# Optimization experiments

Hardware: AMD Instinct MI355X
Metric: run time of the kernel (lower is better)

## Reference

```python
import jax, jax.numpy as jnp
import numpy as np

EPS = 1e-6  # epsilon used to snap near-zero plane distances (Moller-style robustness)


def _interval(p, d):
    """Interval of the intersection line covered by a triangle.
    p: [..., 3] projections of the 3 vertices onto the intersection-line axis.
    d: [..., 3] signed distances of the 3 vertices to the other triangle's plane.
    Returns (tmin, tmax); invalid (non-straddling) -> (+inf, -inf).
    """
    nxt = jnp.array([1, 2, 0])
    di, dj = d, d[..., nxt]
    pi, pj = p, p[..., nxt]
    # edge crosses the plane iff endpoint distances have opposite signs
    # (or exactly one endpoint lies on the plane)
    valid = (di * dj <= 0) & ~((di == 0) & (dj == 0))
    denom = di - dj
    t = pi + (pj - pi) * di / jnp.where(denom == 0, 1.0, denom)
    tmin = jnp.min(jnp.where(valid, t, jnp.inf), axis=-1)
    tmax = jnp.max(jnp.where(valid, t, -jnp.inf), axis=-1)
    return tmin, tmax


def _pairwise_intersect(T):
    """Moller-style triangle-triangle intersection test for all N^2 pairs.
    T: [N, 3, 3] triangle soup. Returns bool [N, N].
    """
    N = T.shape[0]
    n = jnp.cross(T[:, 1] - T[:, 0], T[:, 2] - T[:, 0])   # [N,3] plane normals
    d = -jnp.sum(n * T[:, 0], axis=-1)                      # [N] plane offsets
    # signed distances: verts of triangle b to plane of triangle u (dv), and vice versa (du)
    dv = jnp.einsum('bvc,nc->bnv', T, n) + d[None, :, None]  # [N,N,3]
    du = jnp.einsum('nvc,bc->bnv', T, n) + d[:, None, None]  # [N,N,3]
    dv = jnp.where(jnp.abs(dv) < EPS, 0.0, dv)
    du = jnp.where(jnp.abs(du) < EPS, 0.0, du)
    # all vertices strictly on one side -> no intersection
    ssv = jnp.all(dv > 0, -1) | jnp.all(dv < 0, -1)
    ssu = jnp.all(du > 0, -1) | jnp.all(du < 0, -1)
    # direction of plane-plane intersection line; project onto its dominant axis
    D = jnp.cross(n[:, None, :], n[None, :, :])              # [N,N,3]
    ax = jnp.argmax(jnp.abs(D), axis=-1)                     # [N,N]
    idx = jnp.broadcast_to(ax[..., None, None], (N, N, 3, 1))
    pv = jnp.take_along_axis(jnp.broadcast_to(T[:, None], (N, N, 3, 3)), idx, -1)[..., 0]
    pu = jnp.take_along_axis(jnp.broadcast_to(T[None, :], (N, N, 3, 3)), idx, -1)[..., 0]
    t0v, t1v = _interval(pv, dv)
    t0u, t1u = _interval(pu, du)
    overlap = jnp.maximum(t0v, t0u) <= jnp.minimum(t1v, t1u)
    return ~ssv & ~ssu & overlap


def setup_inputs() -> dict:
    key = jax.random.key(0)
    triangles = jax.random.normal(key, (2048, 3, 3), dtype=jnp.float32)
    return {"triangles": triangles}


def reference(triangles):
    # CPU extension produces the strictly-upper-triangular pairwise matrix;
    # the torch wrapper symmetrizes it and adds the identity.
    N = triangles.shape[0]
    M = _pairwise_intersect(triangles).astype(jnp.float32)
    S = jnp.triu(M, 1)
    return S + S.T + jnp.eye(N, dtype=jnp.float32)
```

## Files before the change

### kernel.cpp

```cpp
#include <hip/hip_runtime.h>
#include <math.h>


static constexpr float EPS_SNAP = 1e-6f;
static constexpr int TS = 32;

__device__ __forceinline__ float snapz(float x) {
    return (fabsf(x) < EPS_SNAP) ? 0.0f : x;
}

__device__ __forceinline__ void tri_interval(const float p[3], const float d[3],
                                             float& tmin, float& tmax) {
#pragma clang fp contract(off)
    tmin = INFINITY;
    tmax = -INFINITY;
#pragma unroll
    for (int e = 0; e < 3; ++e) {
        const int i0 = e;
        const int i1 = (e + 1) % 3;
        const float di = d[i0], dj = d[i1];
        const float pi = p[i0], pj = p[i1];
        const bool valid = (di * dj <= 0.0f) && !((di == 0.0f) && (dj == 0.0f));
        const float denom = di - dj;
        const float dsafe = (denom == 0.0f) ? 1.0f : denom;
        const float t = pi + ((pj - pi) * di) / dsafe;
        if (valid) {
            tmin = fminf(tmin, t);
            tmax = fmaxf(tmax, t);
        }
    }
}

__global__ __launch_bounds__(256) void plane_kernel(
    const float* __restrict__ tri, float4* __restrict__ planes, int n)
{
#pragma clang fp contract(off)
    const int i = blockIdx.x * 256 + threadIdx.x;
    if (i >= n) return;
    const float* A = tri + (size_t)i * 9;
    float Av[9];
#pragma unroll
    for (int k = 0; k < 9; ++k) Av[k] = A[k];
    const float e1x = Av[3] - Av[0], e1y = Av[4] - Av[1], e1z = Av[5] - Av[2];
    const float e2x = Av[6] - Av[0], e2y = Av[7] - Av[1], e2z = Av[8] - Av[2];
    const float nx = e1y * e2z - e1z * e2y;
    const float ny = e1z * e2x - e1x * e2z;
    const float nz = e1x * e2y - e1y * e2x;
    const float d = -(((nx * Av[0]) + (ny * Av[1])) + (nz * Av[2]));
    planes[i] = make_float4(nx, ny, nz, d);
}

__global__ __launch_bounds__(256) void tile_kernel(
    const float* __restrict__ tri, const float4* __restrict__ planes,
    float* __restrict__ out, int n)
{
#pragma clang fp contract(off)
    const int tc = blockIdx.x, tr = blockIdx.y;
    if (tr > tc) return;
    const int C = tc * TS, R = tr * TS;

    __shared__ float As[TS][13];
    __shared__ float Sres[TS][TS + 1];

    const int tx = threadIdx.x;
    const int t = threadIdx.y * 32 + tx;

    if (t < TS) {
        const float* a = tri + (size_t)(R + t) * 9;
#pragma unroll
        for (int k = 0; k < 9; ++k) As[t][k] = a[k];
        const float4 p = planes[R + t];
        As[t][9] = p.x; As[t][10] = p.y; As[t][11] = p.z; As[t][12] = p.w;
    }

    const int j = C + tx;
    const float* b = tri + (size_t)j * 9;
    float Bv[9];
#pragma unroll
    for (int k = 0; k < 9; ++k) Bv[k] = b[k];
    const float4 pb = planes[j];
    const float nbx = pb.x, nby = pb.y, nbz = pb.z, db = pb.w;

    __syncthreads();

#pragma unroll
    for (int kk = 0; kk < 4; ++kk) {
        const int r = threadIdx.y + 8 * kk;
        const int i = R + r;

        float Av[9];
#pragma unroll
        for (int k = 0; k < 9; ++k) Av[k] = As[r][k];
        const float nax = As[r][9], nay = As[r][10], naz = As[r][11], da = As[r][12];

        float dv[3], du[3];
#pragma unroll
        for (int v = 0; v < 3; ++v) {
            dv[v] = snapz((((Av[3 * v] * nbx) + (Av[3 * v + 1] * nby)) + (Av[3 * v + 2] * nbz)) + db);
            du[v] = snapz((((Bv[3 * v] * nax) + (Bv[3 * v + 1] * nay)) + (Bv[3 * v + 2] * naz)) + da);
        }

        const bool ssv = (dv[0] > 0.0f && dv[1] > 0.0f && dv[2] > 0.0f) ||
                         (dv[0] < 0.0f && dv[1] < 0.0f && dv[2] < 0.0f);
        const bool ssu = (du[0] > 0.0f && du[1] > 0.0f && du[2] > 0.0f) ||
                         (du[0] < 0.0f && du[1] < 0.0f && du[2] < 0.0f);

        const float Dx = nay * nbz - naz * nby;
        const float Dy = naz * nbx - nax * nbz;
        const float Dz = nax * nby - nay * nbx;
        const float m0 = fabsf(Dx), m1 = fabsf(Dy), m2 = fabsf(Dz);
        int axm = 0;
        float mm = m0;
        if (m1 > mm) { axm = 1; mm = m1; }
        if (m2 > mm) { axm = 2; }

        float pv[3], pu[3];
#pragma unroll
        for (int v = 0; v < 3; ++v) {
            pv[v] = (axm == 0) ? Av[3 * v] : ((axm == 1) ? Av[3 * v + 1] : Av[3 * v + 2]);
            pu[v] = (axm == 0) ? Bv[3 * v] : ((axm == 1) ? Bv[3 * v + 1] : Bv[3 * v + 2]);
        }

        float t0v, t1v, t0u, t1u;
        tri_interval(pv, dv, t0v, t1v);
        tri_interval(pu, du, t0u, t1u);

        const bool overlap = fmaxf(t0v, t0u) <= fminf(t1v, t1u);
        const bool hit = (!ssv) && (!ssu) && overlap;

        float res = hit ? 1.0f : 0.0f;
        if (i == j) res = 1.0f;
        Sres[r][tx] = res;
    }

    __syncthreads();

    {
        const int row = t >> 3;
        const int c4 = (t & 7) * 4;
        float4 v;
        v.x = Sres[row][c4 + 0]; v.y = Sres[row][c4 + 1];
        v.z = Sres[row][c4 + 2]; v.w = Sres[row][c4 + 3];
        *(float4*)&out[(size_t)(R + row) * n + C + c4] = v;
        if (tr != tc) {
            float4 w;
            w.x = Sres[c4 + 0][row]; w.y = Sres[c4 + 1][row];
            w.z = Sres[c4 + 2][row]; w.w = Sres[c4 + 3][row];
            *(float4*)&out[(size_t)(C + row) * n + R + c4] = w;
        }
    }
}

extern "C" void kernel_launch(void* const* d_in, const int* in_sizes, int n_in,
                              void* d_out, int out_size, void* d_ws, size_t ws_size,
                              hipStream_t stream) {
    const float* tri = (const float*)d_in[0];
    float* out = (float*)d_out;
    const int n = in_sizes[0] / 9;
    float4* planes = (float4*)d_ws;

    plane_kernel<<<(n + 255) / 256, 256, 0, stream>>>(tri, planes, n);

    dim3 block(32, 8);
    dim3 grid(n / TS, n / TS);
    tile_kernel<<<grid, block, 0, stream>>>(tri, planes, out, n);
}
```

Baseline: 78.63 us.

## Use 32x32 thread blocks with one pair per thread and scalar stores

Each tile block grows from 32x8 threads looping over four rows to 32x32 threads that each handle a single triangle pair. The direct tile is stored with per-thread scalar writes, and the mirrored tile goes through shared memory only on off-diagonal blocks. The aim is more parallelism per block and no per-thread row loop, at the cost of each thread redundantly loading B triangle data, scalar instead of float4 stores, and a __syncthreads inside a block-uniform branch.

Result: slower. 80.22 us (+2.0%).

```diff
diff --git a/kernel.cpp b/kernel.cpp
--- a/kernel.cpp
+++ b/kernel.cpp
@@ -50,7 +50,7 @@
     planes[i] = make_float4(nx, ny, nz, d);
 }
 
-__global__ __launch_bounds__(256) void tile_kernel(
+__global__ __launch_bounds__(1024) void tile_kernel(
     const float* __restrict__ tri, const float4* __restrict__ planes,
     float* __restrict__ out, int n)
 {
@@ -63,14 +63,14 @@
     __shared__ float Sres[TS][TS + 1];
 
     const int tx = threadIdx.x;
-    const int t = threadIdx.y * 32 + tx;
+    const int ty = threadIdx.y;
 
-    if (t < TS) {
-        const float* a = tri + (size_t)(R + t) * 9;
+    if (ty == 0) {
+        const float* a = tri + (size_t)(R + tx) * 9;
 #pragma unroll
-        for (int k = 0; k < 9; ++k) As[t][k] = a[k];
-        const float4 p = planes[R + t];
-        As[t][9] = p.x; As[t][10] = p.y; As[t][11] = p.z; As[t][12] = p.w;
+        for (int k = 0; k < 9; ++k) As[tx][k] = a[k];
+        const float4 p = planes[R + tx];
+        As[tx][9] = p.x; As[tx][10] = p.y; As[tx][11] = p.z; As[tx][12] = p.w;
     }
 
     const int j = C + tx;
@@ -83,71 +83,56 @@
 
     __syncthreads();
 
+    const int i = R + ty;
+    float Av[9];
 #pragma unroll
-    for (int kk = 0; kk < 4; ++kk) {
-        const int r = threadIdx.y + 8 * kk;
-        const int i = R + r;
+    for (int k = 0; k < 9; ++k) Av[k] = As[ty][k];
+    const float nax = As[ty][9], nay = As[ty][10], naz = As[ty][11], da = As[ty][12];
 
-        float Av[9];
+    float dv[3], du[3];
 #pragma unroll
-        for (int k = 0; k < 9; ++k) Av[k] = As[r][k];
-        const float nax = As[r][9], nay = As[r][10], naz = As[r][11], da = As[r][12];
-
-        float dv[3], du[3];
-#pragma unroll
-        for (int v = 0; v < 3; ++v) {
-            dv[v] = snapz((((Av[3 * v] * nbx) + (Av[3 * v + 1] * nby)) + (Av[3 * v + 2] * nbz)) + db);
-            du[v] = snapz((((Bv[3 * v] * nax) + (Bv[3 * v + 1] * nay)) + (Bv[3 * v + 2] * naz)) + da);
-        }
-
-        const bool ssv = (dv[0] > 0.0f && dv[1] > 0.0f && dv[2] > 0.0f) ||
-                         (dv[0] < 0.0f && dv[1] < 0.0f && dv[2] < 0.0f);
-        const bool ssu = (du[0] > 0.0f && du[1] > 0.0f && du[2] > 0.0f) ||
-                         (du[0] < 0.0f && du[1] < 0.0f && du[2] < 0.0f);
-
-        const float Dx = nay * nbz - naz * nby;
-        const float Dy = naz * nbx - nax * nbz;
-        const float Dz = nax * nby - nay * nbx;
-        const float m0 = fabsf(Dx), m1 = fabsf(Dy), m2 = fabsf(Dz);
-        int axm = 0;
-        float mm = m0;
-        if (m1 > mm) { axm = 1; mm = m1; }
-        if (m2 > mm) { axm = 2; }
-
-        float pv[3], pu[3];
-#pragma unroll
-        for (int v = 0; v < 3; ++v) {
-            pv[v] = (axm == 0) ? Av[3 * v] : ((axm == 1) ? Av[3 * v + 1] : Av[3 * v + 2]);
-            pu[v] = (axm == 0) ? Bv[3 * v] : ((axm == 1) ? Bv[3 * v + 1] : Bv[3 * v + 2]);
-        }
-
-        float t0v, t1v, t0u, t1u;
-        tri_interval(pv, dv, t0v, t1v);
-        tri_interval(pu, du, t0u, t1u);
-
-        const bool overlap = fmaxf(t0v, t0u) <= fminf(t1v, t1u);
-        const bool hit = (!ssv) && (!ssu) && overlap;
-
-        float res = hit ? 1.0f : 0.0f;
-        if (i == j) res = 1.0f;
-        Sres[r][tx] = res;
+    for (int v = 0; v < 3; ++v) {
+        dv[v] = snapz((((Av[3 * v] * nbx) + (Av[3 * v + 1] * nby)) + (Av[3 * v + 2] * nbz)) + db);
+        du[v] = snapz((((Bv[3 * v] * nax) + (Bv[3 * v + 1] * nay)) + (Bv[3 * v + 2] * naz)) + da);
     }
 
-    __syncthreads();
+    const bool ssv = (dv[0] > 0.0f && dv[1] > 0.0f && dv[2] > 0.0f) ||
+                     (dv[0] < 0.0f && dv[1] < 0.0f && dv[2] < 0.0f);
+    const bool ssu = (du[0] > 0.0f && du[1] > 0.0f && du[2] > 0.0f) ||
+                     (du[0] < 0.0f && du[1] < 0.0f && du[2] < 0.0f);
 
-    {
-        const int row = t >> 3;
-        const int c4 = (t & 7) * 4;
-        float4 v;
-        v.x = Sres[row][c4 + 0]; v.y = Sres[row][c4 + 1];
-        v.z = Sres[row][c4 + 2]; v.w = Sres[row][c4 + 3];
-        *(float4*)&out[(size_t)(R + row) * n + C + c4] = v;
-        if (tr != tc) {
-            float4 w;
-            w.x = Sres[c4 + 0][row]; w.y = Sres[c4 + 1][row];
-            w.z = Sres[c4 + 2][row]; w.w = Sres[c4 + 3][row];
-            *(float4*)&out[(size_t)(C + row) * n + R + c4] = w;
-        }
+    const float Dx = nay * nbz - naz * nby;
+    const float Dy = naz * nbx - nax * nbz;
+    const float Dz = nax * nby - nay * nbx;
+    const float m0 = fabsf(Dx), m1 = fabsf(Dy), m2 = fabsf(Dz);
+    int axm = 0;
+    float mm = m0;
+    if (m1 > mm) { axm = 1; mm = m1; }
+    if (m2 > mm) { axm = 2; }
+
+    float pv[3], pu[3];
+#pragma unroll
+    for (int v = 0; v < 3; ++v) {
+        pv[v] = (axm == 0) ? Av[3 * v] : ((axm == 1) ? Av[3 * v + 1] : Av[3 * v + 2]);
+        pu[v] = (axm == 0) ? Bv[3 * v] : ((axm == 1) ? Bv[3 * v + 1] : Bv[3 * v + 2]);
+    }
+
+    float t0v, t1v, t0u, t1u;
+    tri_interval(pv, dv, t0v, t1v);
+    tri_interval(pu, du, t0u, t1u);
+
+    const bool overlap = fmaxf(t0v, t0u) <= fminf(t1v, t1u);
+    const bool hit = (!ssv) && (!ssu) && overlap;
+
+    float res = hit ? 1.0f : 0.0f;
+    if (i == j) res = 1.0f;
+
+    out[(size_t)i * n + j] = res;
+
+    if (tr != tc) {
+        Sres[ty][tx] = res;
+        __syncthreads();
+        out[(size_t)(C + ty) * n + (R + tx)] = Sres[tx][ty];
     }
 }
 
@@ -161,7 +146,7 @@
 
     plane_kernel<<<(n + 255) / 256, 256, 0, stream>>>(tri, planes, n);
 
-    dim3 block(32, 8);
+    dim3 block(TS, TS);
     dim3 grid(n / TS, n / TS);
     tile_kernel<<<grid, block, 0, stream>>>(tri, planes, out, n);
 }
```

## Fuse plane computation, launch only upper tiles, compact survivors before interval test

Applied to the files above, without the earlier changes.

Plane normals are now computed inside the tile kernel from triangles staged in shared memory, so the separate plane kernel launch goes away. The grid launches only upper-triangular tiles, decoding the tile index with a loop, which removes the empty blocks that used to exit early. A cheap same-side rejection pass uses ballot and a shared atomic to compact surviving pairs into a queue. The full interval test then runs only on those survivors, reducing divergent work, at the cost of extra barriers, atomics and shared memory.

Measured after the change: 73.88 us. 6.0% less time.

```diff
diff --git a/kernel.cpp b/kernel.cpp
--- a/kernel.cpp
+++ b/kernel.cpp
@@ -31,79 +31,124 @@
     }
 }
 
-__global__ __launch_bounds__(256) void plane_kernel(
-    const float* __restrict__ tri, float4* __restrict__ planes, int n)
+__global__ __launch_bounds__(256, 4) void tile_kernel(
+    const float* __restrict__ tri, float* __restrict__ out, int n)
 {
 #pragma clang fp contract(off)
-    const int i = blockIdx.x * 256 + threadIdx.x;
-    if (i >= n) return;
-    const float* A = tri + (size_t)i * 9;
-    float Av[9];
-#pragma unroll
-    for (int k = 0; k < 9; ++k) Av[k] = A[k];
-    const float e1x = Av[3] - Av[0], e1y = Av[4] - Av[1], e1z = Av[5] - Av[2];
-    const float e2x = Av[6] - Av[0], e2y = Av[7] - Av[1], e2z = Av[8] - Av[2];
-    const float nx = e1y * e2z - e1z * e2y;
-    const float ny = e1z * e2x - e1x * e2z;
-    const float nz = e1x * e2y - e1y * e2x;
-    const float d = -(((nx * Av[0]) + (ny * Av[1])) + (nz * Av[2]));
-    planes[i] = make_float4(nx, ny, nz, d);
-}
-
-__global__ __launch_bounds__(256) void tile_kernel(
-    const float* __restrict__ tri, const float4* __restrict__ planes,
-    float* __restrict__ out, int n)
-{
-#pragma clang fp contract(off)
-    const int tc = blockIdx.x, tr = blockIdx.y;
-    if (tr > tc) return;
-    const int C = tc * TS, R = tr * TS;
-
-    __shared__ float As[TS][13];
+    const int nt = n / TS;
+    int k = blockIdx.x, tr = 0;
+    while (k >= nt - tr) { k -= nt - tr; ++tr; }
+    const int tc = tr + k;
+    const int R = tr * TS, C = tc * TS;
+
+    __shared__ float Asf[TS * 12];
+    __shared__ float Bsf[TS * 12];
+    __shared__ float4 Apl[TS], Bpl[TS];
     __shared__ float Sres[TS][TS + 1];
+    __shared__ unsigned short qbuf[TS * TS];
+    __shared__ int s_cnt;
 
     const int tx = threadIdx.x;
-    const int t = threadIdx.y * 32 + tx;
-
-    if (t < TS) {
-        const float* a = tri + (size_t)(R + t) * 9;
-#pragma unroll
-        for (int k = 0; k < 9; ++k) As[t][k] = a[k];
-        const float4 p = planes[R + t];
-        As[t][9] = p.x; As[t][10] = p.y; As[t][11] = p.z; As[t][12] = p.w;
-    }
-
-    const int j = C + tx;
-    const float* b = tri + (size_t)j * 9;
+    const int ty = threadIdx.y;
+    const int t = ty * TS + tx;
+    const int lane = t & 63;
+
+    if (t == 0) s_cnt = 0;
+    for (int g = t; g < TS * 9; g += 256) {
+        const int a = g / 9, c9 = g - a * 9;
+        Asf[a * 12 + c9] = tri[(size_t)R * 9 + g];
+        Bsf[a * 12 + c9] = tri[(size_t)C * 9 + g];
+    }
+    for (int g = t; g < TS * (TS + 1); g += 256) ((float*)Sres)[g] = 0.0f;
+    __syncthreads();
+
+    if (t < 2 * TS) {
+        const float* V = (t < TS) ? &Asf[t * 12] : &Bsf[(t - TS) * 12];
+        const float e1x = V[3] - V[0], e1y = V[4] - V[1], e1z = V[5] - V[2];
+        const float e2x = V[6] - V[0], e2y = V[7] - V[1], e2z = V[8] - V[2];
+        const float nx = e1y * e2z - e1z * e2y;
+        const float ny = e1z * e2x - e1x * e2z;
+        const float nz = e1x * e2y - e1y * e2x;
+        const float d = -(((nx * V[0]) + (ny * V[1])) + (nz * V[2]));
+        if (t < TS) Apl[t] = make_float4(nx, ny, nz, d);
+        else        Bpl[t - TS] = make_float4(nx, ny, nz, d);
+    }
+    if (tr == tc && t < TS) Sres[t][t] = 1.0f;
+    __syncthreads();
+
     float Bv[9];
-#pragma unroll
-    for (int k = 0; k < 9; ++k) Bv[k] = b[k];
-    const float4 pb = planes[j];
-    const float nbx = pb.x, nby = pb.y, nbz = pb.z, db = pb.w;
-
-    __syncthreads();
-
-#pragma unroll
+    {
+        const float4 b0 = *(const float4*)&Bsf[tx * 12];
+        const float4 b1 = *(const float4*)&Bsf[tx * 12 + 4];
+        const float4 b2 = *(const float4*)&Bsf[tx * 12 + 8];
+        Bv[0] = b0.x; Bv[1] = b0.y; Bv[2] = b0.z; Bv[3] = b0.w;
+        Bv[4] = b1.x; Bv[5] = b1.y; Bv[6] = b1.z; Bv[7] = b1.w;
+        Bv[8] = b2.x;
+    }
+    const float4 pb = Bpl[tx];
+
     for (int kk = 0; kk < 4; ++kk) {
-        const int r = threadIdx.y + 8 * kk;
-        const int i = R + r;
-
-        float Av[9];
-#pragma unroll
-        for (int k = 0; k < 9; ++k) Av[k] = As[r][k];
-        const float nax = As[r][9], nay = As[r][10], naz = As[r][11], da = As[r][12];
+        const int r = ty + 8 * kk;
+        const float4 a0 = *(const float4*)&Asf[r * 12];
+        const float4 a1 = *(const float4*)&Asf[r * 12 + 4];
+        const float4 a2 = *(const float4*)&Asf[r * 12 + 8];
+        const float4 pa = Apl[r];
+        const float dv0 = snapz((((a0.x * pb.x) + (a0.y * pb.y)) + (a0.z * pb.z)) + pb.w);
+        const float dv1 = snapz((((a0.w * pb.x) + (a1.x * pb.y)) + (a1.y * pb.z)) + pb.w);
+        const float dv2 = snapz((((a1.z * pb.x) + (a1.w * pb.y)) + (a2.x * pb.z)) + pb.w);
+        const float du0 = snapz((((Bv[0] * pa.x) + (Bv[1] * pa.y)) + (Bv[2] * pa.z)) + pa.w);
+        const float du1 = snapz((((Bv[3] * pa.x) + (Bv[4] * pa.y)) + (Bv[5] * pa.z)) + pa.w);
+        const float du2 = snapz((((Bv[6] * pa.x) + (Bv[7] * pa.y)) + (Bv[8] * pa.z)) + pa.w);
+        const float mnv = fminf(fminf(dv0, dv1), dv2), mxv = fmaxf(fmaxf(dv0, dv1), dv2);
+        const float mnu = fminf(fminf(du0, du1), du2), mxu = fmaxf(fmaxf(du0, du1), du2);
+        const bool ssv = (mnv > 0.0f) || (mxv < 0.0f);
+        const bool ssu = (mnu > 0.0f) || (mxu < 0.0f);
+        const bool surv = !ssv && !ssu && ((R + r) != (C + tx));
+        const unsigned long long m = __ballot(surv);
+        int wb = 0;
+        if (lane == 0) {
+            const int wcnt = __popcll(m);
+            if (wcnt) wb = atomicAdd(&s_cnt, wcnt);
+        }
+        wb = __shfl(wb, 0);
+        if (surv) {
+            const int pos = wb + __popcll(m & ((1ull << lane) - 1ull));
+            qbuf[pos] = (unsigned short)((r << 5) | tx);
+        }
+    }
+    __syncthreads();
+
+    const int total = s_cnt;
+    for (int q = t; q < total; q += 256) {
+        const int e = qbuf[q];
+        const int r = e >> 5, c = e & 31;
+
+        float Av[9], Bw[9];
+        {
+            const float4 a0 = *(const float4*)&Asf[r * 12];
+            const float4 a1 = *(const float4*)&Asf[r * 12 + 4];
+            const float4 a2 = *(const float4*)&Asf[r * 12 + 8];
+            Av[0] = a0.x; Av[1] = a0.y; Av[2] = a0.z; Av[3] = a0.w;
+            Av[4] = a1.x; Av[5] = a1.y; Av[6] = a1.z; Av[7] = a1.w;
+            Av[8] = a2.x;
+            const float4 b0 = *(const float4*)&Bsf[c * 12];
+            const float4 b1 = *(const float4*)&Bsf[c * 12 + 4];
+            const float4 b2 = *(const float4*)&Bsf[c * 12 + 8];
+            Bw[0] = b0.x; Bw[1] = b0.y; Bw[2] = b0.z; Bw[3] = b0.w;
+            Bw[4] = b1.x; Bw[5] = b1.y; Bw[6] = b1.z; Bw[7] = b1.w;
+            Bw[8] = b2.x;
+        }
+        const float4 pa = Apl[r];
+        const float4 pq = Bpl[c];
+        const float nax = pa.x, nay = pa.y, naz = pa.z, da = pa.w;
+        const float nbx = pq.x, nby = pq.y, nbz = pq.z, db = pq.w;
 
         float dv[3], du[3];
 #pragma unroll
         for (int v = 0; v < 3; ++v) {
             dv[v] = snapz((((Av[3 * v] * nbx) + (Av[3 * v + 1] * nby)) + (Av[3 * v + 2] * nbz)) + db);
-            du[v] = snapz((((Bv[3 * v] * nax) + (Bv[3 * v + 1] * nay)) + (Bv[3 * v + 2] * naz)) + da);
-        }
-
-        const bool ssv = (dv[0] > 0.0f && dv[1] > 0.0f && dv[2] > 0.0f) ||
-                         (dv[0] < 0.0f && dv[1] < 0.0f && dv[2] < 0.0f);
-        const bool ssu = (du[0] > 0.0f && du[1] > 0.0f && du[2] > 0.0f) ||
-                         (du[0] < 0.0f && du[1] < 0.0f && du[2] < 0.0f);
+            du[v] = snapz((((Bw[3 * v] * nax) + (Bw[3 * v + 1] * nay)) + (Bw[3 * v + 2] * naz)) + da);
+        }
 
         const float Dx = nay * nbz - naz * nby;
         const float Dy = naz * nbx - nax * nbz;
@@ -118,7 +163,7 @@
 #pragma unroll
         for (int v = 0; v < 3; ++v) {
             pv[v] = (axm == 0) ? Av[3 * v] : ((axm == 1) ? Av[3 * v + 1] : Av[3 * v + 2]);
-            pu[v] = (axm == 0) ? Bv[3 * v] : ((axm == 1) ? Bv[3 * v + 1] : Bv[3 * v + 2]);
+            pu[v] = (axm == 0) ? Bw[3 * v] : ((axm == 1) ? Bw[3 * v + 1] : Bw[3 * v + 2]);
         }
 
         float t0v, t1v, t0u, t1u;
@@ -126,13 +171,8 @@
         tri_interval(pu, du, t0u, t1u);
 
         const bool overlap = fmaxf(t0v, t0u) <= fminf(t1v, t1u);
-        const bool hit = (!ssv) && (!ssu) && overlap;
-
-        float res = hit ? 1.0f : 0.0f;
-        if (i == j) res = 1.0f;
-        Sres[r][tx] = res;
-    }
-
+        Sres[r][c] = overlap ? 1.0f : 0.0f;
+    }
     __syncthreads();
 
     {
@@ -157,11 +197,9 @@
     const float* tri = (const float*)d_in[0];
     float* out = (float*)d_out;
     const int n = in_sizes[0] / 9;
-    float4* planes = (float4*)d_ws;
-
-    plane_kernel<<<(n + 255) / 256, 256, 0, stream>>>(tri, planes, n);
-
-    dim3 block(32, 8);
-    dim3 grid(n / TS, n / TS);
-    tile_kernel<<<grid, block, 0, stream>>>(tri, planes, out, n);
-}
+
+    const int nt = n / TS;
+    const int nblocks = nt * (nt + 1) / 2;
+    dim3 block(TS, 8);
+    tile_kernel<<<nblocks, block, 0, stream>>>(tri, out, n);
+}
```
